# Performance work log

Hardware: AMD Instinct MI355X
Metric: run time of the kernel (lower is better)

## Reference

```python
import jax, jax.numpy as jnp
import numpy as np


def _cdist(x, y):
    # Euclidean (L2) distance matrix, matching torch.cdist default p=2.
    # x: [B,N,D], y: [B,M,D] -> [B,N,M]
    x2 = jnp.sum(x * x, axis=-1, keepdims=True)          # [B,N,1]
    y2 = jnp.sum(y * y, axis=-1, keepdims=True)          # [B,M,1]
    d2 = x2 + jnp.swapaxes(y2, -1, -2) - 2.0 * jnp.einsum('bnd,bmd->bnm', x, y)
    return jnp.sqrt(jnp.maximum(d2, 0.0))


def setup_inputs() -> dict:
    key = jax.random.key(0)
    k1, k2, k3 = jax.random.split(key, 3)
    B, N, G, D = 1, 8192, 2048, 64
    expression = jax.random.normal(k1, (B, N, G), dtype=jnp.float32)
    encoding = jax.random.normal(k2, (B, N, D), dtype=jnp.float32)
    quality = jax.random.normal(k3, (B, N, 1), dtype=jnp.float32)
    return {"expression": expression, "encoding": encoding, "quality": quality}


def reference(expression, encoding, quality):
    # scores[b,i,j] = -||enc_i - enc_j|| + quality[b,j]
    scores = -_cdist(encoding, encoding) + jnp.swapaxes(quality, -1, -2)  # [B,N,N]
    similarity = jax.nn.softmax(scores, axis=-1)
    return similarity @ expression  # [B,N,G]
```

## Files before the change

### kernel.cpp

```cpp
#include <hip/hip_runtime.h>
#include <hip/hip_bf16.h>


typedef __attribute__((ext_vector_type(8))) short bf16x8;
typedef __attribute__((ext_vector_type(4))) float f32x4;
typedef __attribute__((ext_vector_type(16))) float f32x16;

constexpr int N_ = 8192;
constexpr int G_ = 2048;
constexpr int D_ = 64;

__device__ __forceinline__ unsigned short f32_to_bf16(float f) {
  unsigned u = __builtin_bit_cast(unsigned, f);
  u = (u + 0x7FFFu + ((u >> 16) & 1u)) >> 16;
  return (unsigned short)u;
}
__device__ __forceinline__ float bf16_to_f32(unsigned short h) {
  unsigned u = ((unsigned)h) << 16;
  return __builtin_bit_cast(float, u);
}

typedef __attribute__((address_space(1))) const unsigned int glob_u32;
typedef __attribute__((address_space(3))) unsigned int lds_u32;
__device__ __forceinline__ void gload_lds16(const void* g, void* l) {
  __builtin_amdgcn_global_load_lds((glob_u32*)g, (lds_u32*)l, 16, 0, 0);
}

__global__ void prep_kernel(const float* __restrict__ enc,
                            const float* __restrict__ quality,
                            float* __restrict__ norms,
                            float2* __restrict__ nq,
                            unsigned short* __restrict__ encb) {
  int row = blockIdx.x * blockDim.x + threadIdx.x;
  if (row >= N_) return;
  const float* r = enc + (size_t)row * D_;
  float n = 0.f;
#pragma unroll
  for (int k = 0; k < D_; k += 4) {
    float4 v = *(const float4*)(r + k);
    n += v.x * v.x + v.y * v.y + v.z * v.z + v.w * v.w;
    ushort4 h;
    h.x = f32_to_bf16(v.x); h.y = f32_to_bf16(v.y);
    h.z = f32_to_bf16(v.z); h.w = f32_to_bf16(v.w);
    *(ushort4*)(encb + (size_t)row * D_ + k) = h;
  }
  norms[row] = n;
  nq[row] = make_float2(n, quality[row]);
}

__global__ void etrans_kernel(const float* __restrict__ E,
                              unsigned short* __restrict__ ET) {
  __shared__ __align__(16) unsigned short t[64 * 72];
  int j0 = blockIdx.x * 64;
  int g0 = blockIdx.y * 64;
  int tid = threadIdx.x;
#pragma unroll
  for (int it = 0; it < 4; ++it) {
    int r = it * 16 + (tid >> 4);
    int c4 = tid & 15;
    float4 v = *(const float4*)(E + (size_t)(j0 + r) * G_ + g0 + c4 * 4);
    t[(c4 * 4 + 0) * 72 + r] = f32_to_bf16(v.x);
    t[(c4 * 4 + 1) * 72 + r] = f32_to_bf16(v.y);
    t[(c4 * 4 + 2) * 72 + r] = f32_to_bf16(v.z);
    t[(c4 * 4 + 3) * 72 + r] = f32_to_bf16(v.w);
  }
  __syncthreads();
#pragma unroll
  for (int it = 0; it < 2; ++it) {
    int g = it * 32 + (tid >> 3);
    int ch = tid & 7;
    bf16x8 v = *(const bf16x8*)(&t[g * 72 + ch * 8]);
    *(bf16x8*)(ET + (size_t)(g0 + g) * N_ + j0 + ch * 8) = v;
  }
}

__global__ __launch_bounds__(256)
void pk_kernel(const unsigned short* __restrict__ encb,
               const float* __restrict__ norms,
               const float2* __restrict__ nq,
               unsigned short* __restrict__ P,
               float* __restrict__ lpart) {
  __shared__ __align__(16) unsigned short p_lds[64 * 72];

  const int tid = threadIdx.x;
  const int wave = tid >> 6;
  const int lane = tid & 63;
  const int quad = lane >> 4;
  const int l15 = lane & 15;

  const int i0 = blockIdx.y * 64;
  const int jbase = blockIdx.x * 1024;
  const int irow_a = i0 + 16 * wave + l15;
  const int iloc_c = 16 * wave + quad * 4;
  const int irow_c = i0 + iloc_c;

  const int srow_loc = 16 * wave + (lane >> 2);

  bf16x8 afrag[2];
#pragma unroll
  for (int ks = 0; ks < 2; ++ks)
    afrag[ks] = *(const bf16x8*)(encb + (size_t)irow_a * 64 + ks * 32 + quad * 8);

  float ni[4];
#pragma unroll
  for (int r = 0; r < 4; ++r) ni[r] = norms[irow_c + r];

  float lsum[4] = {0.f, 0.f, 0.f, 0.f};

  for (int js = 0; js < 16; ++js) {
    const int j0j = jbase + js * 64;
#pragma unroll
    for (int jt = 0; jt < 4; ++jt) {
      const int jrow = j0j + jt * 16 + l15;
      bf16x8 b0 = *(const bf16x8*)(encb + (size_t)jrow * 64 + quad * 8);
      bf16x8 b1 = *(const bf16x8*)(encb + (size_t)jrow * 64 + 32 + quad * 8);
      float2 njq = nq[jrow];
      f32x4 s4 = {0.f, 0.f, 0.f, 0.f};
      s4 = __builtin_amdgcn_mfma_f32_16x16x32_bf16(afrag[0], b0, s4, 0, 0, 0);
      s4 = __builtin_amdgcn_mfma_f32_16x16x32_bf16(afrag[1], b1, s4, 0, 0, 0);
#pragma unroll
      for (int r = 0; r < 4; ++r) {
        float d2 = fmaxf(ni[r] + njq.x - 2.0f * s4[r], 0.f);
        float sc = njq.y - sqrtf(d2);
        if (irow_c + r == jrow) sc = njq.y;
        float p = __expf(sc);
        unsigned short pb = f32_to_bf16(p);
        lsum[r] += bf16_to_f32(pb);
        p_lds[(iloc_c + r) * 72 + jt * 16 + l15] = pb;
      }
    }
    __syncthreads();
#pragma unroll
    for (int k = 0; k < 2; ++k) {
      int c = (lane & 3) + k * 4;
      bf16x8 v = *(const bf16x8*)(&p_lds[srow_loc * 72 + c * 8]);
      *(bf16x8*)(P + (size_t)(i0 + srow_loc) * N_ + j0j + c * 8) = v;
    }
    __syncthreads();
  }
#pragma unroll
  for (int r = 0; r < 4; ++r) {
    float v = lsum[r];
    v += __shfl_xor(v, 1);
    v += __shfl_xor(v, 2);
    v += __shfl_xor(v, 4);
    v += __shfl_xor(v, 8);
    lsum[r] = v;
  }
  if (l15 == 0) {
#pragma unroll
    for (int r = 0; r < 4; ++r)
      lpart[(size_t)blockIdx.x * N_ + irow_c + r] = lsum[r];
  }
}

__global__ void inv_kernel(const float* __restrict__ lpart,
                           float* __restrict__ linv) {
  int i = blockIdx.x * blockDim.x + threadIdx.x;
  if (i >= N_) return;
  float s = 0.f;
#pragma unroll
  for (int c = 0; c < 8; ++c) s += lpart[(size_t)c * N_ + i];
  linv[i] = 1.0f / s;
}

constexpr int GBM = 256, GBN = 256, GBK = 32;
constexpr int GNT = N_ / GBK;
constexpr int SLOT_A = GBM * GBK;
constexpr int SLOT_B = GBN * GBK;
constexpr int SLOT = SLOT_A + SLOT_B;
constexpr int GEMM_LDS_BYTES = 3 * SLOT * 2;

__global__ __launch_bounds__(512, 1)
void gemm8_kernel(const unsigned short* __restrict__ P,
                  const unsigned short* __restrict__ ET,
                  const float* __restrict__ linv,
                  float* __restrict__ out) {
  extern __shared__ __align__(16) unsigned short smem[];

  const int tid = threadIdx.x;
  const int wave = tid >> 6;
  const int lane = tid & 63;
  const int quad = lane >> 4;
  const int l15 = lane & 15;

  const int bid = blockIdx.x;
  const int lg = (bid & 7) * 32 + (bid >> 3);
  const int gx = lg & 7;
  const int gy = lg >> 3;
  const int g0 = gx * GBN;
  const int i0 = gy * GBM;

  const int wm = wave >> 2;
  const int wn = wave & 3;
  const int wrow = wm * 128;
  const int wcol = wn * 64;

  unsigned short* cur = smem;
  unsigned short* nxt = smem + SLOT;
  unsigned short* stg = smem + 2 * SLOT;

  const int strow = tid >> 2;
  const int stch = tid & 3;
  const int rowS0 = strow, rowS1 = 128 + strow;
  const int cs0 = stch ^ ((rowS0 >> 1) & 3);
  const int cs1 = stch ^ ((rowS1 >> 1) & 3);
  const int dA0 = rowS0 * GBK + stch * 8;
  const int dA1 = rowS1 * GBK + stch * 8;
  const int dB0 = SLOT_A + rowS0 * GBK + stch * 8;
  const int dB1 = SLOT_A + rowS1 * GBK + stch * 8;
  const unsigned short* pA0 = P + (size_t)(i0 + rowS0) * N_ + cs0 * 8;
  const unsigned short* pA1 = P + (size_t)(i0 + rowS1) * N_ + cs1 * 8;
  const unsigned short* pB0 = ET + (size_t)(g0 + rowS0) * N_ + cs0 * 8;
  const unsigned short* pB1 = ET + (size_t)(g0 + rowS1) * N_ + cs1 * 8;

  int offA0[4], offA1[4], offB[4];
#pragma unroll
  for (int r = 0; r < 4; ++r) {
    int rowh0 = wrow + r * 16 + l15;
    int rowh1 = wrow + 64 + r * 16 + l15;
    offA0[r] = rowh0 * GBK + (quad ^ ((rowh0 >> 1) & 3)) * 8;
    offA1[r] = rowh1 * GBK + (quad ^ ((rowh1 >> 1) & 3)) * 8;
    int rowb = wcol + r * 16 + l15;
    offB[r] = SLOT_A + rowb * GBK + (quad ^ ((rowb >> 1) & 3)) * 8;
  }

  f32x4 acc[8][4];
#pragma unroll
  for (int a = 0; a < 8; ++a)
#pragma unroll
    for (int b = 0; b < 4; ++b) acc[a][b] = (f32x4){0.f, 0.f, 0.f, 0.f};

  gload_lds16(pA0, cur + dA0);
  gload_lds16(pA1, cur + dA1);
  gload_lds16(pB0, cur + dB0);
  gload_lds16(pB1, cur + dB1);
  gload_lds16(pA0 + GBK, nxt + dA0);
  gload_lds16(pA1 + GBK, nxt + dA1);
  gload_lds16(pB0 + GBK, nxt + dB0);
  gload_lds16(pB1 + GBK, nxt + dB1);
  pA0 += 2 * GBK; pA1 += 2 * GBK; pB0 += 2 * GBK; pB1 += 2 * GBK;
  asm volatile("s_waitcnt vmcnt(4)" ::: "memory");
  __builtin_amdgcn_s_barrier();

  for (int u = 0; u < GNT; ++u) {
    const bool do_stage = (u + 2 < GNT);
    __builtin_amdgcn_sched_barrier(0);
    if (do_stage) {
      gload_lds16(pA0, stg + dA0);
      gload_lds16(pA1, stg + dA1);
      gload_lds16(pB0, stg + dB0);
      gload_lds16(pB1, stg + dB1);
      pA0 += GBK; pA1 += GBK; pB0 += GBK; pB1 += GBK;
    }
    bf16x8 bF[4], aF0[4], aF1[4];
#pragma unroll
    for (int r = 0; r < 4; ++r) bF[r] = *(const bf16x8*)(cur + offB[r]);
#pragma unroll
    for (int r = 0; r < 4; ++r) aF0[r] = *(const bf16x8*)(cur + offA0[r]);
    __builtin_amdgcn_s_setprio(1);
#pragma unroll
    for (int r = 0; r < 4; ++r)
#pragma unroll
      for (int c = 0; c < 4; ++c)
        acc[r][c] = __builtin_amdgcn_mfma_f32_16x16x32_bf16(aF0[r], bF[c], acc[r][c], 0, 0, 0);
#pragma unroll
    for (int r = 0; r < 4; ++r) aF1[r] = *(const bf16x8*)(cur + offA1[r]);
#pragma unroll
    for (int r = 0; r < 4; ++r)
#pragma unroll
      for (int c = 0; c < 4; ++c)
        acc[4 + r][c] = __builtin_amdgcn_mfma_f32_16x16x32_bf16(aF1[r], bF[c], acc[4 + r][c], 0, 0, 0);
    __builtin_amdgcn_s_setprio(0);
    if (do_stage) {
      asm volatile("s_waitcnt vmcnt(4)" ::: "memory");
    } else {
      asm volatile("s_waitcnt vmcnt(0)" ::: "memory");
    }
    __builtin_amdgcn_s_barrier();
    unsigned short* tmp = cur; cur = nxt; nxt = stg; stg = tmp;
  }

#pragma unroll
  for (int rt = 0; rt < 8; ++rt) {
    float lir[4];
#pragma unroll
    for (int r = 0; r < 4; ++r)
      lir[r] = linv[i0 + wrow + rt * 16 + quad * 4 + r];
#pragma unroll
    for (int ct = 0; ct < 4; ++ct)
#pragma unroll
      for (int r = 0; r < 4; ++r) {
        int row = wrow + rt * 16 + quad * 4 + r;
        int col = wcol + ct * 16 + l15;
        out[(size_t)(i0 + row) * G_ + g0 + col] = acc[rt][ct][r] * lir[r];
      }
  }
}

__global__ __launch_bounds__(256, 2)
void gemm_kernel(const unsigned short* __restrict__ P,
                 const unsigned short* __restrict__ ET,
                 const float* __restrict__ linv,
                 float* __restrict__ out) {
  __shared__ __align__(16) unsigned short aT[256 * 64];
  __shared__ __align__(16) unsigned short bT[128 * 64];

  const int tid = threadIdx.x;
  const int wave = tid >> 6;
  const int lane = tid & 63;
  const int quad = lane >> 4;
  const int l15 = lane & 15;

  const int g0 = blockIdx.x * 128;
  const int i0 = blockIdx.y * 256;
  const int wrow = (wave >> 1) * 128;
  const int wcol = (wave & 1) * 64;

  const int strow = tid >> 3;
  const int stc = tid & 7;

  f32x4 acc[8][4];
#pragma unroll
  for (int a = 0; a < 8; ++a)
#pragma unroll
    for (int b = 0; b < 4; ++b) acc[a][b] = (f32x4){0.f, 0.f, 0.f, 0.f};

  for (int kk = 0; kk < N_; kk += 64) {
#pragma unroll
    for (int s = 0; s < 8; ++s) {
      int row = s * 32 + strow;
      int csrc = stc ^ (row & 7);
      gload_lds16(P + (size_t)(i0 + row) * N_ + kk + csrc * 8,
                  &aT[row * 64 + stc * 8]);
    }
#pragma unroll
    for (int s = 0; s < 4; ++s) {
      int row = s * 32 + strow;
      int csrc = stc ^ (row & 7);
      gload_lds16(ET + (size_t)(g0 + row) * N_ + kk + csrc * 8,
                  &bT[row * 64 + stc * 8]);
    }
    __syncthreads();
#pragma unroll
    for (int ks = 0; ks < 2; ++ks) {
      const int swzk = ((ks * 4 + quad) ^ (l15 & 7)) * 8;
      bf16x8 bF[4];
#pragma unroll
      for (int ct = 0; ct < 4; ++ct)
        bF[ct] = *(const bf16x8*)(&bT[(wcol + ct * 16 + l15) * 64 + swzk]);
#pragma unroll
      for (int rt = 0; rt < 8; ++rt) {
        bf16x8 aF = *(const bf16x8*)(&aT[(wrow + rt * 16 + l15) * 64 + swzk]);
#pragma unroll
        for (int ct = 0; ct < 4; ++ct)
          acc[rt][ct] = __builtin_amdgcn_mfma_f32_16x16x32_bf16(aF, bF[ct], acc[rt][ct], 0, 0, 0);
      }
    }
    __syncthreads();
  }

#pragma unroll
  for (int rt = 0; rt < 8; ++rt) {
    float lir[4];
#pragma unroll
    for (int r = 0; r < 4; ++r)
      lir[r] = linv[i0 + wrow + rt * 16 + quad * 4 + r];
#pragma unroll
    for (int ct = 0; ct < 4; ++ct)
#pragma unroll
      for (int r = 0; r < 4; ++r) {
        int row = wrow + rt * 16 + quad * 4 + r;
        int col = wcol + ct * 16 + l15;
        out[(size_t)(i0 + row) * G_ + g0 + col] = acc[rt][ct][r] * lir[r];
      }
  }
}

__global__ __launch_bounds__(256, 2)
void fused_kernel(const unsigned short* __restrict__ encb,
                  const float* __restrict__ norms,
                  const float2* __restrict__ nq,
                  const unsigned short* __restrict__ ET,
                  float* __restrict__ out) {
  __shared__ __align__(16) unsigned short p_lds[128 * 72];
  __shared__ __align__(16) unsigned short e_lds[256 * 72];
  __shared__ float linv_lds[128];

  const int tid = threadIdx.x;
  const int wave = tid >> 6;
  const int lane = tid & 63;
  const int quad = lane >> 4;
  const int l15 = lane & 15;
  const int half = lane >> 5;
  const int l31 = lane & 31;

  const int gt = blockIdx.x & 7;
  const int it = blockIdx.x >> 3;
  const int i0 = it * 128;
  const int g0 = gt * 256;

  const int srow = 32 * wave;
  const int wr = wave >> 1, wc = wave & 1;
  const int prow = 64 * wr;
  const int pcol = 128 * wc;

  bf16x8 afrag[2][2];
#pragma unroll
  for (int rt = 0; rt < 2; ++rt)
#pragma unroll
    for (int ks = 0; ks < 2; ++ks)
      afrag[rt][ks] = *(const bf16x8*)(encb +
          (size_t)(i0 + srow + rt * 16 + l15) * 64 + ks * 32 + quad * 8);

  float ni[2][4];
#pragma unroll
  for (int rt = 0; rt < 2; ++rt)
#pragma unroll
    for (int r = 0; r < 4; ++r)
      ni[rt][r] = norms[i0 + srow + rt * 16 + quad * 4 + r];

  float lsum[2][4] = {};
  f32x16 acc[2][4];
#pragma unroll
  for (int a = 0; a < 2; ++a)
#pragma unroll
    for (int b = 0; b < 4; ++b)
#pragma unroll
      for (int e = 0; e < 16; ++e) acc[a][b][e] = 0.f;

  for (int j0j = 0; j0j < N_; j0j += 64) {
#pragma unroll
    for (int s = 0; s < 8; ++s) {
      int g = s * 32 + (tid >> 3);
      int ch = tid & 7;
      bf16x8 v = *(const bf16x8*)(ET + (size_t)(g0 + g) * N_ + j0j + ch * 8);
      *(bf16x8*)(&e_lds[g * 72 + ch * 8]) = v;
    }
#pragma unroll
    for (int jt = 0; jt < 4; ++jt) {
      const int jrow = j0j + jt * 16 + l15;
      bf16x8 b0 = *(const bf16x8*)(encb + (size_t)jrow * 64 + quad * 8);
      bf16x8 b1 = *(const bf16x8*)(encb + (size_t)jrow * 64 + 32 + quad * 8);
      float2 njq = nq[jrow];
#pragma unroll
      for (int rt = 0; rt < 2; ++rt) {
        f32x4 s4 = {0.f, 0.f, 0.f, 0.f};
        s4 = __builtin_amdgcn_mfma_f32_16x16x32_bf16(afrag[rt][0], b0, s4, 0, 0, 0);
        s4 = __builtin_amdgcn_mfma_f32_16x16x32_bf16(afrag[rt][1], b1, s4, 0, 0, 0);
#pragma unroll
        for (int r = 0; r < 4; ++r) {
          int i_loc = srow + rt * 16 + quad * 4 + r;
          float d2 = fmaxf(ni[rt][r] + njq.x - 2.0f * s4[r], 0.f);
          float sc = njq.y - sqrtf(d2);
          if (i0 + i_loc == jrow) sc = njq.y;
          float p = __expf(sc);
          unsigned short pb = f32_to_bf16(p);
          lsum[rt][r] += bf16_to_f32(pb);
          p_lds[i_loc * 72 + jt * 16 + l15] = pb;
        }
      }
    }
    __syncthreads();
#pragma unroll
    for (int ks = 0; ks < 4; ++ks) {
      bf16x8 pa0 = *(const bf16x8*)(&p_lds[(prow + l31) * 72 + ks * 16 + half * 8]);
      bf16x8 pa1 = *(const bf16x8*)(&p_lds[(prow + 32 + l31) * 72 + ks * 16 + half * 8]);
#pragma unroll
      for (int ct = 0; ct < 4; ++ct) {
        bf16x8 eb = *(const bf16x8*)(&e_lds[(pcol + ct * 32 + l31) * 72 + ks * 16 + half * 8]);
        acc[0][ct] = __builtin_amdgcn_mfma_f32_32x32x16_bf16(pa0, eb, acc[0][ct], 0, 0, 0);
        acc[1][ct] = __builtin_amdgcn_mfma_f32_32x32x16_bf16(pa1, eb, acc[1][ct], 0, 0, 0);
      }
    }
    __syncthreads();
  }

#pragma unroll
  for (int rt = 0; rt < 2; ++rt)
#pragma unroll
    for (int r = 0; r < 4; ++r) {
      float v = lsum[rt][r];
      v += __shfl_xor(v, 1);
      v += __shfl_xor(v, 2);
      v += __shfl_xor(v, 4);
      v += __shfl_xor(v, 8);
      lsum[rt][r] = v;
    }
  if (l15 == 0) {
#pragma unroll
    for (int rt = 0; rt < 2; ++rt)
#pragma unroll
      for (int r = 0; r < 4; ++r)
        linv_lds[srow + rt * 16 + quad * 4 + r] = 1.0f / lsum[rt][r];
  }
  __syncthreads();

#pragma unroll
  for (int rt2 = 0; rt2 < 2; ++rt2)
#pragma unroll
    for (int ct = 0; ct < 4; ++ct)
#pragma unroll
      for (int e = 0; e < 16; ++e) {
        int row = prow + rt2 * 32 + (e & 3) + 8 * (e >> 2) + 4 * half;
        int col = pcol + ct * 32 + l31;
        out[(size_t)(i0 + row) * G_ + g0 + col] = acc[rt2][ct][e] * linv_lds[row];
      }
}

extern "C" void kernel_launch(void* const* d_in, const int* in_sizes, int n_in,
                              void* d_out, int out_size, void* d_ws, size_t ws_size,
                              hipStream_t stream) {
  const float* expr = (const float*)d_in[0];
  const float* enc  = (const float*)d_in[1];
  const float* qual = (const float*)d_in[2];
  float* out = (float*)d_out;

  char* ws = (char*)d_ws;
  const size_t off_norms = 0;
  const size_t off_nq    = 32768;
  const size_t off_lpart = 98304;
  const size_t off_linv  = 360448;
  const size_t off_encb  = 393216;
  const size_t off_ET    = 1441792;
  const size_t off_P     = 34996224;
  const size_t need      = off_P + (size_t)N_ * N_ * 2;

  static bool smem_init = false;
  static bool smem_ok = false;
  if (!smem_init) {
    smem_init = true;
    hipError_t e = hipFuncSetAttribute(
        reinterpret_cast<const void*>(gemm8_kernel),
        hipFuncAttributeMaxDynamicSharedMemorySize, GEMM_LDS_BYTES);
    smem_ok = (e == hipSuccess);
  }

  if (ws_size >= need) {
    float* norms         = (float*)(ws + off_norms);
    float2* nqp          = (float2*)(ws + off_nq);
    float* lpart         = (float*)(ws + off_lpart);
    float* linv          = (float*)(ws + off_linv);
    unsigned short* encb = (unsigned short*)(ws + off_encb);
    unsigned short* ET   = (unsigned short*)(ws + off_ET);
    unsigned short* P    = (unsigned short*)(ws + off_P);

    prep_kernel<<<dim3(N_ / 256), dim3(256), 0, stream>>>(enc, qual, norms, nqp, encb);
    etrans_kernel<<<dim3(N_ / 64, G_ / 64), dim3(256), 0, stream>>>(expr, ET);
    pk_kernel<<<dim3(8, N_ / 64), dim3(256), 0, stream>>>(encb, norms, nqp, P, lpart);
    inv_kernel<<<dim3(N_ / 256), dim3(256), 0, stream>>>(lpart, linv);
    if (smem_ok) {
      gemm8_kernel<<<dim3((N_ / GBM) * (G_ / GBN)), dim3(512), GEMM_LDS_BYTES, stream>>>(
          P, ET, linv, out);
    } else {
      gemm_kernel<<<dim3(G_ / 128, N_ / 256), dim3(256), 0, stream>>>(P, ET, linv, out);
    }
  } else {
    float* norms         = (float*)ws;
    float2* nqp          = (float2*)(ws + 32768);
    unsigned short* encb = (unsigned short*)(ws + 98304);
    unsigned short* ET   = (unsigned short*)(ws + 1146880);
    prep_kernel<<<dim3(N_ / 256), dim3(256), 0, stream>>>(enc, qual, norms, nqp, encb);
    etrans_kernel<<<dim3(N_ / 64, G_ / 64), dim3(256), 0, stream>>>(expr, ET);
    fused_kernel<<<dim3((N_ / 128) * (G_ / 256)), dim3(256), 0, stream>>>(encb, norms, nqp, ET, out);
  }
}
```

Baseline: 427.2 us.

## Software-pipeline LDS fragment loads across K steps with register double buffering

```diff
diff --git a/kernel.cpp b/kernel.cpp
--- a/kernel.cpp
+++ b/kernel.cpp
@@ -171,7 +171,7 @@
 constexpr int SLOT = SLOT_A + SLOT_B;
 constexpr int GEMM_LDS_BYTES = 3 * SLOT * 2;
 
-__global__ __launch_bounds__(512, 1)
+__global__ __launch_bounds__(512, 2)
 void gemm8_kernel(const unsigned short* __restrict__ P,
                   const unsigned short* __restrict__ ET,
                   const float* __restrict__ linv,
@@ -196,34 +196,22 @@
   const int wrow = wm * 128;
   const int wcol = wn * 64;
 
-  unsigned short* cur = smem;
-  unsigned short* nxt = smem + SLOT;
-  unsigned short* stg = smem + 2 * SLOT;
+  unsigned short* s0 = smem;
+  unsigned short* s1 = smem + SLOT;
+  unsigned short* s2 = smem + 2 * SLOT;
 
   const int strow = tid >> 2;
   const int stch = tid & 3;
-  const int rowS0 = strow, rowS1 = 128 + strow;
-  const int cs0 = stch ^ ((rowS0 >> 1) & 3);
-  const int cs1 = stch ^ ((rowS1 >> 1) & 3);
-  const int dA0 = rowS0 * GBK + stch * 8;
-  const int dA1 = rowS1 * GBK + stch * 8;
-  const int dB0 = SLOT_A + rowS0 * GBK + stch * 8;
-  const int dB1 = SLOT_A + rowS1 * GBK + stch * 8;
-  const unsigned short* pA0 = P + (size_t)(i0 + rowS0) * N_ + cs0 * 8;
-  const unsigned short* pA1 = P + (size_t)(i0 + rowS1) * N_ + cs1 * 8;
-  const unsigned short* pB0 = ET + (size_t)(g0 + rowS0) * N_ + cs0 * 8;
-  const unsigned short* pB1 = ET + (size_t)(g0 + rowS1) * N_ + cs1 * 8;
-
-  int offA0[4], offA1[4], offB[4];
-#pragma unroll
-  for (int r = 0; r < 4; ++r) {
-    int rowh0 = wrow + r * 16 + l15;
-    int rowh1 = wrow + 64 + r * 16 + l15;
-    offA0[r] = rowh0 * GBK + (quad ^ ((rowh0 >> 1) & 3)) * 8;
-    offA1[r] = rowh1 * GBK + (quad ^ ((rowh1 >> 1) & 3)) * 8;
-    int rowb = wcol + r * 16 + l15;
-    offB[r] = SLOT_A + rowb * GBK + (quad ^ ((rowb >> 1) & 3)) * 8;
-  }
+  const int csw = stch ^ ((strow >> 1) & 3);
+  const int dstA = strow * GBK + stch * 8;
+  unsigned gA0 = (unsigned)(i0 + strow) * N_ + csw * 8;
+  unsigned gA1 = (unsigned)(i0 + 128 + strow) * N_ + csw * 8;
+  unsigned gB0 = (unsigned)(g0 + strow) * N_ + csw * 8;
+  unsigned gB1 = (unsigned)(g0 + 128 + strow) * N_ + csw * 8;
+
+  const int fswz = (quad ^ ((l15 >> 1) & 3)) * 8;
+  const int aBase = (wrow + l15) * GBK + fswz;
+  const int bBase = SLOT_A + (wcol + l15) * GBK + fswz;
 
   f32x4 acc[8][4];
 #pragma unroll
@@ -231,54 +219,91 @@
 #pragma unroll
     for (int b = 0; b < 4; ++b) acc[a][b] = (f32x4){0.f, 0.f, 0.f, 0.f};
 
-  gload_lds16(pA0, cur + dA0);
-  gload_lds16(pA1, cur + dA1);
-  gload_lds16(pB0, cur + dB0);
-  gload_lds16(pB1, cur + dB1);
-  gload_lds16(pA0 + GBK, nxt + dA0);
-  gload_lds16(pA1 + GBK, nxt + dA1);
-  gload_lds16(pB0 + GBK, nxt + dB0);
-  gload_lds16(pB1 + GBK, nxt + dB1);
-  pA0 += 2 * GBK; pA1 += 2 * GBK; pB0 += 2 * GBK; pB1 += 2 * GBK;
+  bf16x8 fa0[8], fb0[4], fa1[8], fb1[4];
+
+  gload_lds16(P + gA0, s0 + dstA);
+  gload_lds16(P + gA1, s0 + dstA + 4096);
+  gload_lds16(ET + gB0, s0 + SLOT_A + dstA);
+  gload_lds16(ET + gB1, s0 + SLOT_A + dstA + 4096);
+  gA0 += GBK; gA1 += GBK; gB0 += GBK; gB1 += GBK;
+  gload_lds16(P + gA0, s1 + dstA);
+  gload_lds16(P + gA1, s1 + dstA + 4096);
+  gload_lds16(ET + gB0, s1 + SLOT_A + dstA);
+  gload_lds16(ET + gB1, s1 + SLOT_A + dstA + 4096);
+  gA0 += GBK; gA1 += GBK; gB0 += GBK; gB1 += GBK;
   asm volatile("s_waitcnt vmcnt(4)" ::: "memory");
   __builtin_amdgcn_s_barrier();
-
-  for (int u = 0; u < GNT; ++u) {
-    const bool do_stage = (u + 2 < GNT);
-    __builtin_amdgcn_sched_barrier(0);
-    if (do_stage) {
-      gload_lds16(pA0, stg + dA0);
-      gload_lds16(pA1, stg + dA1);
-      gload_lds16(pB0, stg + dB0);
-      gload_lds16(pB1, stg + dB1);
-      pA0 += GBK; pA1 += GBK; pB0 += GBK; pB1 += GBK;
-    }
-    bf16x8 bF[4], aF0[4], aF1[4];
-#pragma unroll
-    for (int r = 0; r < 4; ++r) bF[r] = *(const bf16x8*)(cur + offB[r]);
-#pragma unroll
-    for (int r = 0; r < 4; ++r) aF0[r] = *(const bf16x8*)(cur + offA0[r]);
+  {
+    const unsigned short* pa = s0 + aBase;
+    const unsigned short* pb = s0 + bBase;
+#pragma unroll
+    for (int r = 0; r < 4; ++r) fb0[r] = *(const bf16x8*)(pb + r * 512);
+#pragma unroll
+    for (int r = 0; r < 4; ++r) fa0[r] = *(const bf16x8*)(pa + r * 512);
+#pragma unroll
+    for (int r = 0; r < 4; ++r) fa0[4 + r] = *(const bf16x8*)(pa + 2048 + r * 512);
+  }
+  gload_lds16(P + gA0, s2 + dstA);
+  gload_lds16(P + gA1, s2 + dstA + 4096);
+  gload_lds16(ET + gB0, s2 + SLOT_A + dstA);
+  gload_lds16(ET + gB1, s2 + SLOT_A + dstA + 4096);
+  gA0 += GBK; gA1 += GBK; gB0 += GBK; gB1 += GBK;
+  asm volatile("s_waitcnt vmcnt(4)" ::: "memory");
+  asm volatile("s_waitcnt lgkmcnt(0)" ::: "memory");
+  __builtin_amdgcn_s_barrier();
+  __builtin_amdgcn_sched_barrier(0);
+
+  unsigned short* cur = s1;
+  unsigned short* nxt = s2;
+  unsigned short* stg = s0;
+
+  int u = 0;
+  auto body = [&](bf16x8(&faC)[8], bf16x8(&fbC)[4],
+                  bf16x8(&faN)[8], bf16x8(&fbN)[4]) {
+    if (u < GNT - 3) {
+      gload_lds16(P + gA0, stg + dstA);
+      gload_lds16(P + gA1, stg + dstA + 4096);
+      gload_lds16(ET + gB0, stg + SLOT_A + dstA);
+      gload_lds16(ET + gB1, stg + SLOT_A + dstA + 4096);
+      gA0 += GBK; gA1 += GBK; gB0 += GBK; gB1 += GBK;
+    }
+    if (u < GNT - 1) {
+      const unsigned short* pa = cur + aBase;
+      const unsigned short* pb = cur + bBase;
+#pragma unroll
+      for (int r = 0; r < 4; ++r) fbN[r] = *(const bf16x8*)(pb + r * 512);
+#pragma unroll
+      for (int r = 0; r < 4; ++r) faN[r] = *(const bf16x8*)(pa + r * 512);
+#pragma unroll
+      for (int r = 0; r < 4; ++r) faN[4 + r] = *(const bf16x8*)(pa + 2048 + r * 512);
+    }
     __builtin_amdgcn_s_setprio(1);
 #pragma unroll
     for (int r = 0; r < 4; ++r)
 #pragma unroll
       for (int c = 0; c < 4; ++c)
-        acc[r][c] = __builtin_amdgcn_mfma_f32_16x16x32_bf16(aF0[r], bF[c], acc[r][c], 0, 0, 0);
-#pragma unroll
-    for (int r = 0; r < 4; ++r) aF1[r] = *(const bf16x8*)(cur + offA1[r]);
+        acc[r][c] = __builtin_amdgcn_mfma_f32_16x16x32_bf16(faC[r], fbC[c], acc[r][c], 0, 0, 0);
 #pragma unroll
     for (int r = 0; r < 4; ++r)
 #pragma unroll
       for (int c = 0; c < 4; ++c)
-        acc[4 + r][c] = __builtin_amdgcn_mfma_f32_16x16x32_bf16(aF1[r], bF[c], acc[4 + r][c], 0, 0, 0);
+        acc[4 + r][c] = __builtin_amdgcn_mfma_f32_16x16x32_bf16(faC[4 + r], fbC[c], acc[4 + r][c], 0, 0, 0);
     __builtin_amdgcn_s_setprio(0);
-    if (do_stage) {
+    asm volatile("s_waitcnt lgkmcnt(0)" ::: "memory");
+    if (u < GNT - 3) {
       asm volatile("s_waitcnt vmcnt(4)" ::: "memory");
     } else {
       asm volatile("s_waitcnt vmcnt(0)" ::: "memory");
     }
     __builtin_amdgcn_s_barrier();
-    unsigned short* tmp = cur; cur = nxt; nxt = stg; stg = tmp;
+    __builtin_amdgcn_sched_barrier(0);
+    unsigned short* t_ = cur; cur = nxt; nxt = stg; stg = t_;
+    ++u;
+  };
+
+  for (int it = 0; it < GNT / 2; ++it) {
+    body(fa0, fb0, fa1, fb1);
+    body(fa1, fb1, fa0, fb0);
   }
 
 #pragma unroll
```

Result: faster. 411.4 us (-3.7%).

## Restructure PV GEMM to BK=64 double buffer with register-prefetched fragments

Applied to the files above, without the earlier changes.

```diff
diff --git a/kernel.cpp b/kernel.cpp
--- a/kernel.cpp
+++ b/kernel.cpp
@@ -164,14 +164,13 @@
   linv[i] = 1.0f / s;
 }
 
-constexpr int GBM = 256, GBN = 256, GBK = 32;
+constexpr int GBM = 256, GBN = 256, GBK = 64;
 constexpr int GNT = N_ / GBK;
 constexpr int SLOT_A = GBM * GBK;
-constexpr int SLOT_B = GBN * GBK;
-constexpr int SLOT = SLOT_A + SLOT_B;
-constexpr int GEMM_LDS_BYTES = 3 * SLOT * 2;
-
-__global__ __launch_bounds__(512, 1)
+constexpr int SLOT = 2 * SLOT_A;
+constexpr int GEMM_LDS_BYTES = 2 * SLOT * 2;
+
+__global__ __launch_bounds__(512, 2)
 void gemm8_kernel(const unsigned short* __restrict__ P,
                   const unsigned short* __restrict__ ET,
                   const float* __restrict__ linv,
@@ -196,34 +195,28 @@
   const int wrow = wm * 128;
   const int wcol = wn * 64;
 
-  unsigned short* cur = smem;
-  unsigned short* nxt = smem + SLOT;
-  unsigned short* stg = smem + 2 * SLOT;
-
-  const int strow = tid >> 2;
-  const int stch = tid & 3;
-  const int rowS0 = strow, rowS1 = 128 + strow;
-  const int cs0 = stch ^ ((rowS0 >> 1) & 3);
-  const int cs1 = stch ^ ((rowS1 >> 1) & 3);
-  const int dA0 = rowS0 * GBK + stch * 8;
-  const int dA1 = rowS1 * GBK + stch * 8;
-  const int dB0 = SLOT_A + rowS0 * GBK + stch * 8;
-  const int dB1 = SLOT_A + rowS1 * GBK + stch * 8;
-  const unsigned short* pA0 = P + (size_t)(i0 + rowS0) * N_ + cs0 * 8;
-  const unsigned short* pA1 = P + (size_t)(i0 + rowS1) * N_ + cs1 * 8;
-  const unsigned short* pB0 = ET + (size_t)(g0 + rowS0) * N_ + cs0 * 8;
-  const unsigned short* pB1 = ET + (size_t)(g0 + rowS1) * N_ + cs1 * 8;
-
-  int offA0[4], offA1[4], offB[4];
-#pragma unroll
-  for (int r = 0; r < 4; ++r) {
-    int rowh0 = wrow + r * 16 + l15;
-    int rowh1 = wrow + 64 + r * 16 + l15;
-    offA0[r] = rowh0 * GBK + (quad ^ ((rowh0 >> 1) & 3)) * 8;
-    offA1[r] = rowh1 * GBK + (quad ^ ((rowh1 >> 1) & 3)) * 8;
-    int rowb = wcol + r * 16 + l15;
-    offB[r] = SLOT_A + rowb * GBK + (quad ^ ((rowb >> 1) & 3)) * 8;
-  }
+  unsigned short* b0 = smem;
+  unsigned short* b1 = smem + SLOT;
+
+  const int strow = tid >> 3;
+  const int stch = tid & 7;
+  const int csw = stch ^ (strow & 7);
+  const int dstT = tid * 8;
+  unsigned gSA0 = (unsigned)(i0 + 0 * 64 + strow) * N_ + csw * 8;
+  unsigned gSA1 = (unsigned)(i0 + 1 * 64 + strow) * N_ + csw * 8;
+  unsigned gSA2 = (unsigned)(i0 + 2 * 64 + strow) * N_ + csw * 8;
+  unsigned gSA3 = (unsigned)(i0 + 3 * 64 + strow) * N_ + csw * 8;
+  unsigned gSB0 = (unsigned)(g0 + 0 * 64 + strow) * N_ + csw * 8;
+  unsigned gSB1 = (unsigned)(g0 + 1 * 64 + strow) * N_ + csw * 8;
+  unsigned gSB2 = (unsigned)(g0 + 2 * 64 + strow) * N_ + csw * 8;
+  unsigned gSB3 = (unsigned)(g0 + 3 * 64 + strow) * N_ + csw * 8;
+
+  const int sw0 = (quad ^ (l15 & 7)) * 8;
+  const int sw1 = ((4 + quad) ^ (l15 & 7)) * 8;
+  const int aOff0 = (wrow + l15) * 64 + sw0;
+  const int aOff1 = (wrow + l15) * 64 + sw1;
+  const int bOff0 = SLOT_A + (wcol + l15) * 64 + sw0;
+  const int bOff1 = SLOT_A + (wcol + l15) * 64 + sw1;
 
   f32x4 acc[8][4];
 #pragma unroll
@@ -231,55 +224,74 @@
 #pragma unroll
     for (int b = 0; b < 4; ++b) acc[a][b] = (f32x4){0.f, 0.f, 0.f, 0.f};
 
-  gload_lds16(pA0, cur + dA0);
-  gload_lds16(pA1, cur + dA1);
-  gload_lds16(pB0, cur + dB0);
-  gload_lds16(pB1, cur + dB1);
-  gload_lds16(pA0 + GBK, nxt + dA0);
-  gload_lds16(pA1 + GBK, nxt + dA1);
-  gload_lds16(pB0 + GBK, nxt + dB0);
-  gload_lds16(pB1 + GBK, nxt + dB1);
-  pA0 += 2 * GBK; pA1 += 2 * GBK; pB0 += 2 * GBK; pB1 += 2 * GBK;
-  asm volatile("s_waitcnt vmcnt(4)" ::: "memory");
+  bf16x8 faX[8], fbX[4], faY[8], fbY[4];
+
+#define STAGE8(dst)                                            \
+  do {                                                         \
+    gload_lds16(P + gSA0, (dst) + 0 * 4096 + dstT);            \
+    gload_lds16(P + gSA1, (dst) + 1 * 4096 + dstT);            \
+    gload_lds16(P + gSA2, (dst) + 2 * 4096 + dstT);            \
+    gload_lds16(P + gSA3, (dst) + 3 * 4096 + dstT);            \
+    gload_lds16(ET + gSB0, (dst) + SLOT_A + 0 * 4096 + dstT);  \
+    gload_lds16(ET + gSB1, (dst) + SLOT_A + 1 * 4096 + dstT);  \
+    gload_lds16(ET + gSB2, (dst) + SLOT_A + 2 * 4096 + dstT);  \
+    gload_lds16(ET + gSB3, (dst) + SLOT_A + 3 * 4096 + dstT);  \
+    gSA0 += GBK; gSA1 += GBK; gSA2 += GBK; gSA3 += GBK;        \
+    gSB0 += GBK; gSB1 += GBK; gSB2 += GBK; gSB3 += GBK;        \
+  } while (0)
+
+  STAGE8(b0);
+  STAGE8(b1);
+  asm volatile("s_waitcnt vmcnt(8)" ::: "memory");
   __builtin_amdgcn_s_barrier();
+  {
+    const unsigned short* pb = b0;
+#pragma unroll
+    for (int c = 0; c < 4; ++c) fbX[c] = *(const bf16x8*)(pb + bOff0 + c * 1024);
+#pragma unroll
+    for (int r = 0; r < 8; ++r) faX[r] = *(const bf16x8*)(pb + aOff0 + r * 1024);
+  }
+  asm volatile("s_waitcnt lgkmcnt(0)" ::: "memory");
+  __builtin_amdgcn_sched_barrier(0);
+
+  unsigned short* cur = b0;
+  unsigned short* oth = b1;
 
   for (int u = 0; u < GNT; ++u) {
-    const bool do_stage = (u + 2 < GNT);
+#pragma unroll
+    for (int c = 0; c < 4; ++c) fbY[c] = *(const bf16x8*)(cur + bOff1 + c * 1024);
+#pragma unroll
+    for (int r = 0; r < 8; ++r) faY[r] = *(const bf16x8*)(cur + aOff1 + r * 1024);
+    __builtin_amdgcn_s_setprio(1);
+#pragma unroll
+    for (int r = 0; r < 8; ++r)
+#pragma unroll
+      for (int c = 0; c < 4; ++c)
+        acc[r][c] = __builtin_amdgcn_mfma_f32_16x16x32_bf16(faX[r], fbX[c], acc[r][c], 0, 0, 0);
+    __builtin_amdgcn_s_setprio(0);
+    asm volatile("s_waitcnt lgkmcnt(0)" ::: "memory");
+    asm volatile("s_waitcnt vmcnt(0)" ::: "memory");
+    __builtin_amdgcn_s_barrier();
     __builtin_amdgcn_sched_barrier(0);
-    if (do_stage) {
-      gload_lds16(pA0, stg + dA0);
-      gload_lds16(pA1, stg + dA1);
-      gload_lds16(pB0, stg + dB0);
-      gload_lds16(pB1, stg + dB1);
-      pA0 += GBK; pA1 += GBK; pB0 += GBK; pB1 += GBK;
-    }
-    bf16x8 bF[4], aF0[4], aF1[4];
-#pragma unroll
-    for (int r = 0; r < 4; ++r) bF[r] = *(const bf16x8*)(cur + offB[r]);
-#pragma unroll
-    for (int r = 0; r < 4; ++r) aF0[r] = *(const bf16x8*)(cur + offA0[r]);
+    if (u + 2 < GNT) STAGE8(cur);
+    if (u + 1 < GNT) {
+#pragma unroll
+      for (int c = 0; c < 4; ++c) fbX[c] = *(const bf16x8*)(oth + bOff0 + c * 1024);
+#pragma unroll
+      for (int r = 0; r < 8; ++r) faX[r] = *(const bf16x8*)(oth + aOff0 + r * 1024);
+    }
     __builtin_amdgcn_s_setprio(1);
 #pragma unroll
-    for (int r = 0; r < 4; ++r)
+    for (int r = 0; r < 8; ++r)
 #pragma unroll
       for (int c = 0; c < 4; ++c)
-        acc[r][c] = __builtin_amdgcn_mfma_f32_16x16x32_bf16(aF0[r], bF[c], acc[r][c], 0, 0, 0);
-#pragma unroll
-    for (int r = 0; r < 4; ++r) aF1[r] = *(const bf16x8*)(cur + offA1[r]);
-#pragma unroll
-    for (int r = 0; r < 4; ++r)
-#pragma unroll
-      for (int c = 0; c < 4; ++c)
-        acc[4 + r][c] = __builtin_amdgcn_mfma_f32_16x16x32_bf16(aF1[r], bF[c], acc[4 + r][c], 0, 0, 0);
+        acc[r][c] = __builtin_amdgcn_mfma_f32_16x16x32_bf16(faY[r], fbY[c], acc[r][c], 0, 0, 0);
     __builtin_amdgcn_s_setprio(0);
-    if (do_stage) {
-      asm volatile("s_waitcnt vmcnt(4)" ::: "memory");
-    } else {
-      asm volatile("s_waitcnt vmcnt(0)" ::: "memory");
-    }
-    __builtin_amdgcn_s_barrier();
-    unsigned short* tmp = cur; cur = nxt; nxt = stg; stg = tmp;
-  }
+    asm volatile("s_waitcnt lgkmcnt(0)" ::: "memory");
+    __builtin_amdgcn_sched_barrier(0);
+    unsigned short* t_ = cur; cur = oth; oth = t_;
+  }
+#undef STAGE8
 
 #pragma unroll
   for (int rt = 0; rt < 8; ++rt) {
```

After: 406.4 us. -4.9%, faster.
